# Kernel tuning notes

Hardware: AMD Instinct MI355X
Metric: run time of the kernel (lower is better)

The kernel has to match this reference:

```python
import jax, jax.numpy as jnp
import numpy as np
import math

H = 768      # hidden_size
NH = 12      # num_attention_heads
HS = H // NH # head_size


def setup_inputs() -> dict:
    key = jax.random.key(0)
    ks = jax.random.split(key, 6)
    B, T = 16, 512
    x = jax.random.normal(ks[0], (B, T, H), dtype=jnp.float32)
    attention_mask = jnp.ones((B, T), dtype=jnp.int64)
    s = 0.02
    W_qkv = jax.random.normal(ks[1], (H, 3 * H), dtype=jnp.float32) * s
    b_qkv = jnp.zeros((3 * H,), dtype=jnp.float32)
    W_proj = jax.random.normal(ks[2], (H, H), dtype=jnp.float32) * s
    b_proj = jnp.zeros((H,), dtype=jnp.float32)
    return {"x": x, "attention_mask": attention_mask, "W_qkv": W_qkv,
            "b_qkv": b_qkv, "W_proj": W_proj, "b_proj": b_proj}


def reference(x, attention_mask, W_qkv, b_qkv, W_proj, b_proj):
    B, T, C = x.shape
    qkv = x @ W_qkv + b_qkv                      # [B,T,3H]
    q, k, v = jnp.split(qkv, 3, axis=2)
    # [B,T,H] -> [B,NH,T,HS]
    q = q.reshape(B, T, NH, HS).transpose(0, 2, 1, 3)
    k = k.reshape(B, T, NH, HS).transpose(0, 2, 1, 3)
    v = v.reshape(B, T, NH, HS).transpose(0, 2, 1, 3)
    att = jnp.einsum('bhqd,bhkd->bhqk', q, k) / math.sqrt(HS)
    mask = attention_mask[:, None, None, :]      # [B,1,1,T]
    neg = jnp.finfo(att.dtype).min
    att = jnp.where(mask == 0, neg, att)
    att = jax.nn.softmax(att, axis=-1)
    # dropout is identity in eval / p=0
    y = jnp.einsum('bhqk,bhkd->bhqd', att, v)    # [B,NH,T,HS]
    y = y.transpose(0, 2, 1, 3).reshape(B, T, C)
    y = y @ W_proj + b_proj
    return y
```

## Files before the change

kernel.cpp:

```cpp
#include <hip/hip_runtime.h>


typedef unsigned short u16;
typedef __bf16 bf16x8 __attribute__((ext_vector_type(8)));
typedef float f32x4 __attribute__((ext_vector_type(4)));
typedef unsigned short u16x8 __attribute__((ext_vector_type(8)));

__device__ __forceinline__ u16 f2b(float f) {
  union { float f; unsigned int u; } v; v.f = f;
  unsigned int u = v.u;
  return (u16)((u + 0x7FFFu + ((u >> 16) & 1u)) >> 16);
}

__device__ __forceinline__ u16 f2b_hw(float f) {
  __bf16 b = (__bf16)f;
  return __builtin_bit_cast(u16, b);
}

__device__ __forceinline__ void gload_lds16(const u16* gsrc, u16* ldst) {
  __builtin_amdgcn_global_load_lds(
      (const __attribute__((address_space(1))) void*)gsrc,
      (__attribute__((address_space(3))) void*)ldst,
      16, 0, 0);
}

__device__ __forceinline__ bf16x8 lds_read16(const u16* p) {
  return __builtin_bit_cast(bf16x8, *(const int4*)p);
}


__global__ __launch_bounds__(256) void cvt_x(const float* __restrict__ in,
                                             u16* __restrict__ out, int n8) {
  int i = blockIdx.x * 256 + threadIdx.x;
  if (i >= n8) return;
  float4 v0 = ((const float4*)in)[(size_t)i * 2];
  float4 v1 = ((const float4*)in)[(size_t)i * 2 + 1];
  u16x8 r;
  r[0] = f2b(v0.x); r[1] = f2b(v0.y); r[2] = f2b(v0.z); r[3] = f2b(v0.w);
  r[4] = f2b(v1.x); r[5] = f2b(v1.y); r[6] = f2b(v1.z); r[7] = f2b(v1.w);
  *(u16x8*)(out + (size_t)i * 8) = r;
}

__global__ __launch_bounds__(256) void transpose_cvt(const float* __restrict__ in,
                                                     u16* __restrict__ out, int R, int C) {
  __shared__ float tile[32][33];
  int nbx = C >> 5;
  int bx = blockIdx.x % nbx, by = blockIdx.x / nbx;
  int tx = threadIdx.x & 31, ty = threadIdx.x >> 5;
#pragma unroll
  for (int jj = 0; jj < 32; jj += 8)
    tile[ty + jj][tx] = in[(size_t)(by * 32 + ty + jj) * C + bx * 32 + tx];
  __syncthreads();
#pragma unroll
  for (int jj = 0; jj < 32; jj += 8)
    out[(size_t)(bx * 32 + ty + jj) * R + by * 32 + tx] = f2b(tile[tx][ty + jj]);
}


__global__ __launch_bounds__(256) void gemm_qkv(const u16* __restrict__ A,
                                                const u16* __restrict__ Bt,
                                                const float* __restrict__ bias,
                                                u16* __restrict__ qk,
                                                u16* __restrict__ vt) {
  constexpr int K = 768, KT = 12, NBX = 18;
  __shared__ __align__(16) u16 As[2][128 * 64];
  __shared__ __align__(16) u16 Bs[2][128 * 64];
  const int t = threadIdx.x, l = t & 63, w = t >> 6;
  const int wr = w >> 1, wc = w & 1;
  const int lm = l & 15, g = l >> 4;
  const int cpx = gridDim.x >> 3;
  const int bid = (blockIdx.x & 7) * cpx + (blockIdx.x >> 3);
  const int brow = (bid / NBX) << 7;
  const int bcol = (bid % NBX) << 7;

  f32x4 acc[4][4] = {};

  const int rs = t >> 3, cs = t & 7;
  const int swz = (cs ^ (rs & 7)) * 8;
  const u16* gA = A + (size_t)(brow + rs) * K + swz;
  const u16* gB = Bt + (size_t)(bcol + rs) * K + swz;

  auto stage = [&](int kt, int buf) {
    const int k0 = kt << 6;
#pragma unroll
    for (int p = 0; p < 4; ++p)
      gload_lds16(gA + (size_t)p * 32 * K + k0, As[buf] + p * 2048 + t * 8);
#pragma unroll
    for (int p = 0; p < 4; ++p)
      gload_lds16(gB + (size_t)p * 32 * K + k0, Bs[buf] + p * 2048 + t * 8);
  };

  stage(0, 0);
  __syncthreads();

  for (int kt = 0; kt < KT; ++kt) {
    const int cur = kt & 1;
    if (kt + 1 < KT) stage(kt + 1, cur ^ 1);
    bf16x8 af[4][2], bf_[4][2];
#pragma unroll
    for (int m = 0; m < 4; ++m) {
      int r = wr * 64 + m * 16 + lm;
#pragma unroll
      for (int ks = 0; ks < 2; ++ks)
        af[m][ks] = lds_read16(As[cur] + r * 64 + (((ks * 4 + g) ^ (r & 7)) * 8));
    }
#pragma unroll
    for (int n = 0; n < 4; ++n) {
      int r = wc * 64 + n * 16 + lm;
#pragma unroll
      for (int ks = 0; ks < 2; ++ks)
        bf_[n][ks] = lds_read16(Bs[cur] + r * 64 + (((ks * 4 + g) ^ (r & 7)) * 8));
    }
    __builtin_amdgcn_s_setprio(1);
#pragma unroll
    for (int m = 0; m < 4; ++m)
#pragma unroll
      for (int n = 0; n < 4; ++n)
#pragma unroll
        for (int ks = 0; ks < 2; ++ks)
          acc[m][n] = __builtin_amdgcn_mfma_f32_16x16x32_bf16(af[m][ks], bf_[n][ks],
                                                              acc[m][n], 0, 0, 0);
    __builtin_amdgcn_s_setprio(0);
    __syncthreads();
  }

  if (bcol >= 1536) {
    const int b = brow >> 9;
#pragma unroll
    for (int n = 0; n < 4; ++n) {
      int cv = bcol - 1536 + wc * 64 + n * 16 + lm;
      int hh = cv >> 6, dd = cv & 63;
      float bv = bias[1536 + cv];
      u16* vrow = vt + (((size_t)(b * 12 + hh) * 64 + dd) << 9);
#pragma unroll
      for (int m = 0; m < 4; ++m) {
        int tq = (brow + wr * 64 + m * 16 + g * 4) & 511;
        ushort4 pk;
        pk.x = f2b(acc[m][n][0] + bv);
        pk.y = f2b(acc[m][n][1] + bv);
        pk.z = f2b(acc[m][n][2] + bv);
        pk.w = f2b(acc[m][n][3] + bv);
        *(ushort4*)(vrow + tq) = pk;
      }
    }
  } else {
#pragma unroll
    for (int n = 0; n < 4; ++n) {
      int c = bcol + wc * 64 + n * 16 + lm;
      float bv = bias[c];
#pragma unroll
      for (int m = 0; m < 4; ++m) {
        int rbase = brow + wr * 64 + m * 16 + g * 4;
#pragma unroll
        for (int j = 0; j < 4; ++j)
          qk[(size_t)(rbase + j) * 1536 + c] = f2b(acc[m][n][j] + bv);
      }
    }
  }
}

__global__ __launch_bounds__(256) void gemm_proj(const u16* __restrict__ A,
                                                 const u16* __restrict__ Bt,
                                                 const float* __restrict__ bias,
                                                 float* __restrict__ out) {
  constexpr int K = 768, KT = 12, NBX = 6, N = 768;
  __shared__ __align__(16) u16 As[2][128 * 64];
  __shared__ __align__(16) u16 Bs[2][128 * 64];
  const int t = threadIdx.x, l = t & 63, w = t >> 6;
  const int wr = w >> 1, wc = w & 1;
  const int lm = l & 15, g = l >> 4;
  const int cpx = gridDim.x >> 3;
  const int bid = (blockIdx.x & 7) * cpx + (blockIdx.x >> 3);
  const int brow = (bid / NBX) << 7;
  const int bcol = (bid % NBX) << 7;

  f32x4 acc[4][4] = {};

  const int rs = t >> 3, cs = t & 7;
  const int swz = (cs ^ (rs & 7)) * 8;
  const u16* gA = A + (size_t)(brow + rs) * K + swz;
  const u16* gB = Bt + (size_t)(bcol + rs) * K + swz;

  auto stage = [&](int kt, int buf) {
    const int k0 = kt << 6;
#pragma unroll
    for (int p = 0; p < 4; ++p)
      gload_lds16(gA + (size_t)p * 32 * K + k0, As[buf] + p * 2048 + t * 8);
#pragma unroll
    for (int p = 0; p < 4; ++p)
      gload_lds16(gB + (size_t)p * 32 * K + k0, Bs[buf] + p * 2048 + t * 8);
  };

  stage(0, 0);
  __syncthreads();

  for (int kt = 0; kt < KT; ++kt) {
    const int cur = kt & 1;
    if (kt + 1 < KT) stage(kt + 1, cur ^ 1);
    bf16x8 af[4][2], bf_[4][2];
#pragma unroll
    for (int m = 0; m < 4; ++m) {
      int r = wr * 64 + m * 16 + lm;
#pragma unroll
      for (int ks = 0; ks < 2; ++ks)
        af[m][ks] = lds_read16(As[cur] + r * 64 + (((ks * 4 + g) ^ (r & 7)) * 8));
    }
#pragma unroll
    for (int n = 0; n < 4; ++n) {
      int r = wc * 64 + n * 16 + lm;
#pragma unroll
      for (int ks = 0; ks < 2; ++ks)
        bf_[n][ks] = lds_read16(Bs[cur] + r * 64 + (((ks * 4 + g) ^ (r & 7)) * 8));
    }
    __builtin_amdgcn_s_setprio(1);
#pragma unroll
    for (int m = 0; m < 4; ++m)
#pragma unroll
      for (int n = 0; n < 4; ++n)
#pragma unroll
        for (int ks = 0; ks < 2; ++ks)
          acc[m][n] = __builtin_amdgcn_mfma_f32_16x16x32_bf16(af[m][ks], bf_[n][ks],
                                                              acc[m][n], 0, 0, 0);
    __builtin_amdgcn_s_setprio(0);
    __syncthreads();
  }

#pragma unroll
  for (int n = 0; n < 4; ++n) {
    int c = bcol + wc * 64 + n * 16 + lm;
    float bv = bias[c];
#pragma unroll
    for (int m = 0; m < 4; ++m) {
      int rbase = brow + wr * 64 + m * 16 + g * 4;
#pragma unroll
      for (int j = 0; j < 4; ++j)
        out[(size_t)(rbase + j) * N + c] = acc[m][n][j] + bv;
    }
  }
}


__global__ __launch_bounds__(512) void attn_fused(const u16* __restrict__ qk,
                                                  const u16* __restrict__ vt,
                                                  const int* __restrict__ mask,
                                                  u16* __restrict__ out) {
  __shared__ __align__(16) u16 Ks[2][64 * 64];
  __shared__ __align__(16) u16 Vs[2][64 * 64];
  __shared__ __align__(16) u16 Ps[8][16 * 64];

  const int t = threadIdx.x, l = t & 63, w = t >> 6;
  const int lm = l & 15, g = l >> 4;
  const int bid = (blockIdx.x & 7) * 96 + (blockIdx.x >> 3);
  const int qt = bid & 3;
  const int bh = bid >> 2;
  const int b = bh / 12, h = bh % 12;

  bf16x8 qf[2];
  {
    const u16* qptr = qk + (size_t)(b * 512 + qt * 128 + w * 16 + lm) * 1536 + h * 64;
    qf[0] = *(const bf16x8*)(qptr + g * 8);
    qf[1] = *(const bf16x8*)(qptr + 32 + g * 8);
  }

  unsigned mbits = 0;
#pragma unroll
  for (int kt = 0; kt < 8; ++kt)
#pragma unroll
    for (int n = 0; n < 4; ++n)
      mbits |= (mask[b * 512 + kt * 64 + n * 16 + lm] != 0 ? 1u : 0u) << (kt * 4 + n);

  bf16x8 ones;
  {
    u16x8 o1;
#pragma unroll
    for (int e = 0; e < 8; ++e) o1[e] = 0x3F80;
    ones = __builtin_bit_cast(bf16x8, o1);
  }

  f32x4 o[4] = {};
  f32x4 osum = {};

  const int rk = t >> 3, ck = t & 7;
  const int cswz = ck ^ (rk & 7);
  const u16* srcK = qk + (size_t)(b * 512 + rk) * 1536 + 768 + h * 64 + cswz * 8;
  const u16* srcV = vt + ((size_t)(bh * 64 + rk)) * 512 + cswz * 8;

  auto stage = [&](int kt, int buf) {
    gload_lds16(srcK + (size_t)kt * 64 * 1536, Ks[buf] + t * 8);
    gload_lds16(srcV + kt * 64, Vs[buf] + t * 8);
  };

  stage(0, 0);
  __syncthreads();
  int cur = 0;

  constexpr float SCL = 0.125f * 1.44269504f;

  for (int kt = 0; kt < 8; ++kt) {
    if (kt < 7) stage(kt + 1, cur ^ 1);

    f32x4 s[4] = {};
#pragma unroll
    for (int ds = 0; ds < 2; ++ds) {
#pragma unroll
      for (int n = 0; n < 4; ++n) {
        int r = n * 16 + lm;
        bf16x8 kf = lds_read16(Ks[cur] + r * 64 + (((ds * 4 + g) ^ (r & 7)) * 8));
        s[n] = __builtin_amdgcn_mfma_f32_16x16x32_bf16(qf[ds], kf, s[n], 0, 0, 0);
      }
    }
    u16* pw = Ps[w];
#pragma unroll
    for (int n = 0; n < 4; ++n) {
      bool ok = (mbits >> (kt * 4 + n)) & 1u;
      int key = n * 16 + lm;
#pragma unroll
      for (int j = 0; j < 4; ++j) {
        float sv = ok ? s[n][j] * SCL : -3.0e38f;
        float p = exp2f(sv);
        int q16 = g * 4 + j;
        pw[q16 * 64 + (((key >> 3) ^ (q16 & 7)) * 8) + (key & 7)] = f2b_hw(p);
      }
    }
#pragma unroll
    for (int ks = 0; ks < 2; ++ks) {
      bf16x8 pa = lds_read16(pw + lm * 64 + (((ks * 4 + g) ^ (lm & 7)) * 8));
#pragma unroll
      for (int n = 0; n < 4; ++n) {
        int rd = n * 16 + lm;
        bf16x8 vb = lds_read16(Vs[cur] + rd * 64 + (((ks * 4 + g) ^ (rd & 7)) * 8));
        o[n] = __builtin_amdgcn_mfma_f32_16x16x32_bf16(pa, vb, o[n], 0, 0, 0);
      }
      osum = __builtin_amdgcn_mfma_f32_16x16x32_bf16(pa, ones, osum, 0, 0, 0);
    }
    __syncthreads();
    cur ^= 1;
  }

  float inv[4];
#pragma unroll
  for (int j = 0; j < 4; ++j) inv[j] = 1.0f / osum[j];
#pragma unroll
  for (int n = 0; n < 4; ++n) {
    int d = n * 16 + lm;
#pragma unroll
    for (int j = 0; j < 4; ++j) {
      int tq = qt * 128 + w * 16 + g * 4 + j;
      out[(size_t)(b * 512 + tq) * 768 + h * 64 + d] = f2b_hw(o[n][j] * inv[j]);
    }
  }
}


extern "C" void kernel_launch(void* const* d_in, const int* in_sizes, int n_in,
                              void* d_out, int out_size, void* d_ws, size_t ws_size,
                              hipStream_t stream) {
  const float* x = (const float*)d_in[0];
  const int* mask = (const int*)d_in[1];
  const float* Wqkv = (const float*)d_in[2];
  const float* bqkv = (const float*)d_in[3];
  const float* Wproj = (const float*)d_in[4];
  const float* bproj = (const float*)d_in[5];
  float* out = (float*)d_out;

  char* ws = (char*)d_ws;
  u16* xb     = (u16*)(ws);
  u16* wqkvT  = (u16*)(ws + 12582912);
  u16* wprojT = (u16*)(ws + 16121856);
  u16* qkb    = (u16*)(ws + 17301504);
  u16* vtb    = (u16*)(ws + 42467328);
  u16* attnb  = (u16*)(ws + 55050240);

  cvt_x<<<3072, 256, 0, stream>>>(x, xb, 786432);
  transpose_cvt<<<72 * 24, 256, 0, stream>>>(Wqkv, wqkvT, 768, 2304);
  transpose_cvt<<<24 * 24, 256, 0, stream>>>(Wproj, wprojT, 768, 768);
  gemm_qkv<<<1152, 256, 0, stream>>>(xb, wqkvT, bqkv, qkb, vtb);
  attn_fused<<<768, 512, 0, stream>>>(qkb, vtb, mask, attnb);
  gemm_proj<<<384, 256, 0, stream>>>(attnb, wprojT, bproj, out);
}
```

Baseline: 104.2 us.

## Process two 16-row query tiles per wave in attention with 256-thread blocks

The attention kernel now runs 4 waves per block instead of 8, and each wave handles two 16-row query tiles. Each K and V fragment read from LDS is reused across two MFMAs, halving LDS read traffic per unit of compute. Each thread also issues twice as many global-to-LDS loads per stage. In exchange, each wave holds more accumulators and uses more registers, and there are fewer waves per block to hide latency.

After: 110.3 us. 5.9% more time.

```diff
diff --git a/kernel.cpp b/kernel.cpp
--- a/kernel.cpp
+++ b/kernel.cpp
@@ -240,7 +240,7 @@
 }
 
 
-__global__ __launch_bounds__(512) void attn_fused(const u16* __restrict__ qk,
+__global__ __launch_bounds__(256) void attn_fused(const u16* __restrict__ qk,
                                                   const u16* __restrict__ vt,
                                                   const int* __restrict__ mask,
                                                   u16* __restrict__ out) {
@@ -255,11 +255,14 @@
   const int bh = bid >> 2;
   const int b = bh / 12, h = bh % 12;
 
-  bf16x8 qf[2];
+  bf16x8 qf0[2], qf1[2];
   {
-    const u16* qptr = qk + (size_t)(b * 512 + qt * 128 + w * 16 + lm) * 1536 + h * 64;
-    qf[0] = *(const bf16x8*)(qptr + g * 8);
-    qf[1] = *(const bf16x8*)(qptr + 32 + g * 8);
+    const u16* q0 = qk + (size_t)(b * 512 + qt * 128 + w * 32 + lm) * 1536 + h * 64;
+    const u16* q1 = q0 + (size_t)16 * 1536;
+    qf0[0] = *(const bf16x8*)(q0 + g * 8);
+    qf0[1] = *(const bf16x8*)(q0 + 32 + g * 8);
+    qf1[0] = *(const bf16x8*)(q1 + g * 8);
+    qf1[1] = *(const bf16x8*)(q1 + 32 + g * 8);
   }
 
   unsigned mbits = 0;
@@ -277,8 +280,8 @@
     ones = __builtin_bit_cast(bf16x8, o1);
   }
 
-  f32x4 o[4] = {};
-  f32x4 osum = {};
+  f32x4 o0[4] = {}, o1_[4] = {};
+  f32x4 osum0 = {}, osum1 = {};
 
   const int rk = t >> 3, ck = t & 7;
   const int cswz = ck ^ (rk & 7);
@@ -286,8 +289,11 @@
   const u16* srcV = vt + ((size_t)(bh * 64 + rk)) * 512 + cswz * 8;
 
   auto stage = [&](int kt, int buf) {
-    gload_lds16(srcK + (size_t)kt * 64 * 1536, Ks[buf] + t * 8);
+    const size_t offK = (size_t)kt * 64 * 1536;
+    gload_lds16(srcK + offK, Ks[buf] + t * 8);
+    gload_lds16(srcK + offK + 32 * 1536, Ks[buf] + (t + 256) * 8);
     gload_lds16(srcV + kt * 64, Vs[buf] + t * 8);
+    gload_lds16(srcV + kt * 64 + 32 * 512, Vs[buf] + (t + 256) * 8);
   };
 
   stage(0, 0);
@@ -299,54 +305,63 @@
   for (int kt = 0; kt < 8; ++kt) {
     if (kt < 7) stage(kt + 1, cur ^ 1);
 
-    f32x4 s[4] = {};
+    f32x4 s0[4] = {}, s1[4] = {};
 #pragma unroll
     for (int ds = 0; ds < 2; ++ds) {
 #pragma unroll
       for (int n = 0; n < 4; ++n) {
         int r = n * 16 + lm;
         bf16x8 kf = lds_read16(Ks[cur] + r * 64 + (((ds * 4 + g) ^ (r & 7)) * 8));
-        s[n] = __builtin_amdgcn_mfma_f32_16x16x32_bf16(qf[ds], kf, s[n], 0, 0, 0);
-      }
-    }
-    u16* pw = Ps[w];
+        s0[n] = __builtin_amdgcn_mfma_f32_16x16x32_bf16(qf0[ds], kf, s0[n], 0, 0, 0);
+        s1[n] = __builtin_amdgcn_mfma_f32_16x16x32_bf16(qf1[ds], kf, s1[n], 0, 0, 0);
+      }
+    }
+    u16* pw0 = Ps[w * 2 + 0];
+    u16* pw1 = Ps[w * 2 + 1];
 #pragma unroll
     for (int n = 0; n < 4; ++n) {
       bool ok = (mbits >> (kt * 4 + n)) & 1u;
       int key = n * 16 + lm;
 #pragma unroll
       for (int j = 0; j < 4; ++j) {
-        float sv = ok ? s[n][j] * SCL : -3.0e38f;
-        float p = exp2f(sv);
         int q16 = g * 4 + j;
-        pw[q16 * 64 + (((key >> 3) ^ (q16 & 7)) * 8) + (key & 7)] = f2b_hw(p);
+        int addr = q16 * 64 + (((key >> 3) ^ (q16 & 7)) * 8) + (key & 7);
+        float sv0 = ok ? s0[n][j] * SCL : -3.0e38f;
+        float sv1 = ok ? s1[n][j] * SCL : -3.0e38f;
+        pw0[addr] = f2b_hw(exp2f(sv0));
+        pw1[addr] = f2b_hw(exp2f(sv1));
       }
     }
 #pragma unroll
     for (int ks = 0; ks < 2; ++ks) {
-      bf16x8 pa = lds_read16(pw + lm * 64 + (((ks * 4 + g) ^ (lm & 7)) * 8));
+      int paoff = lm * 64 + (((ks * 4 + g) ^ (lm & 7)) * 8);
+      bf16x8 pa0 = lds_read16(pw0 + paoff);
+      bf16x8 pa1 = lds_read16(pw1 + paoff);
 #pragma unroll
       for (int n = 0; n < 4; ++n) {
         int rd = n * 16 + lm;
         bf16x8 vb = lds_read16(Vs[cur] + rd * 64 + (((ks * 4 + g) ^ (rd & 7)) * 8));
-        o[n] = __builtin_amdgcn_mfma_f32_16x16x32_bf16(pa, vb, o[n], 0, 0, 0);
-      }
-      osum = __builtin_amdgcn_mfma_f32_16x16x32_bf16(pa, ones, osum, 0, 0, 0);
+        o0[n]  = __builtin_amdgcn_mfma_f32_16x16x32_bf16(pa0, vb, o0[n], 0, 0, 0);
+        o1_[n] = __builtin_amdgcn_mfma_f32_16x16x32_bf16(pa1, vb, o1_[n], 0, 0, 0);
+      }
+      osum0 = __builtin_amdgcn_mfma_f32_16x16x32_bf16(pa0, ones, osum0, 0, 0, 0);
+      osum1 = __builtin_amdgcn_mfma_f32_16x16x32_bf16(pa1, ones, osum1, 0, 0, 0);
     }
     __syncthreads();
     cur ^= 1;
   }
 
-  float inv[4];
-#pragma unroll
-  for (int j = 0; j < 4; ++j) inv[j] = 1.0f / osum[j];
+  float inv0[4], inv1[4];
+#pragma unroll
+  for (int j = 0; j < 4; ++j) { inv0[j] = 1.0f / osum0[j]; inv1[j] = 1.0f / osum1[j]; }
 #pragma unroll
   for (int n = 0; n < 4; ++n) {
     int d = n * 16 + lm;
 #pragma unroll
     for (int j = 0; j < 4; ++j) {
-      int tq = qt * 128 + w * 16 + g * 4 + j;
-      out[(size_t)(b * 512 + tq) * 768 + h * 64 + d] = f2b_hw(o[n][j] * inv[j]);
+      int tq0 = qt * 128 + w * 32 + g * 4 + j;
+      out[(size_t)(b * 512 + tq0) * 768 + h * 64 + d] = f2b_hw(o0[n][j] * inv0[j]);
+      out[(size_t)(b * 512 + tq0 + 16) * 768 + h * 64 + d] = f2b_hw(o1_[n][j] * inv1[j]);
     }
   }
 }
@@ -375,6 +390,6 @@
   transpose_cvt<<<72 * 24, 256, 0, stream>>>(Wqkv, wqkvT, 768, 2304);
   transpose_cvt<<<24 * 24, 256, 0, stream>>>(Wproj, wprojT, 768, 768);
   gemm_qkv<<<1152, 256, 0, stream>>>(xb, wqkvT, bqkv, qkb, vtb);
-  attn_fused<<<768, 512, 0, stream>>>(qkb, vtb, mask, attnb);
+  attn_fused<<<768, 256, 0, stream>>>(qkb, vtb, mask, attnb);
   gemm_proj<<<384, 256, 0, stream>>>(attnb, wprojT, bproj, out);
 }
```
